# Performance work log

Measured on AMD Instinct MI355X. Metric: run time of the kernel, lower is better.

## Reference

```python
import jax, jax.numpy as jnp
import numpy as np

B, T, D, H = 1, 4096, 1024, 16
DK = D // H
SCALE = 1.0 / float(np.sqrt(DK))
NEG = -1e9


def setup_inputs() -> dict:
    key = jax.random.key(0)
    k1, k2, k3 = jax.random.split(key, 3)
    x = jax.random.normal(k1, (B, T, D), dtype=jnp.float32)
    # xavier-ish small weights (gain 0.5)
    Wqkv = jax.random.normal(k2, (3 * D, D), dtype=jnp.float32) * 0.02
    Wout = jax.random.normal(k3, (D, D), dtype=jnp.float32) * 0.02
    return {"x": x, "Wqkv": Wqkv, "Wout": Wout}


def reference(x, Wqkv, Wout):
    b, t, d = x.shape
    # QKV projection (no bias): [B,T,3D] -> [3,B,H,T,DK]
    qkv = jnp.einsum('btd,ed->bte', x, Wqkv)
    qkv = qkv.reshape(b, t, 3, H, DK).transpose(2, 0, 3, 1, 4)
    q, k, v = qkv[0], qkv[1], qkv[2]
    # scaled dot-product scores, clamped
    scores = jnp.einsum('bhtd,bhsd->bhts', q, k) * SCALE
    scores = jnp.clip(scores, -10.0, 10.0)
    # causal additive mask (strict upper triangle gets -1e9)
    mask = jnp.triu(jnp.full((t, t), NEG, dtype=scores.dtype), k=1)
    scores = scores + mask[None, None, :, :]
    attn = jax.nn.softmax(scores, axis=-1)  # dropout is identity in eval
    out = jnp.einsum('bhts,bhsd->bhtd', attn, v)
    out = out.transpose(0, 2, 1, 3).reshape(b, t, d)
    return jnp.einsum('btd,ed->bte', out, Wout)
```

## Files before the change

kernel.cpp:

```cpp
#include <hip/hip_runtime.h>

#define T_SEQ   4096
#define D_MODEL 1024
#define NH      16
#define HD      64
#define E3      3072
#define QSCL    0.125f
#define TILEB   (64L*E3)
#define SLOTSZ  16896
#define P0CAP   800

using u32x2  = __attribute__((ext_vector_type(2))) unsigned int;
using u32x4  = __attribute__((ext_vector_type(4))) unsigned int;
using u16x4  = __attribute__((ext_vector_type(4))) unsigned short;
using u16x8  = __attribute__((ext_vector_type(8))) unsigned short;
using u64x2  = __attribute__((ext_vector_type(2))) unsigned long long;
using f32x4  = __attribute__((ext_vector_type(4))) float;
using bf16x8 = __attribute__((ext_vector_type(8))) __bf16;

__device__ __forceinline__ unsigned short f2bf(float f){
  unsigned int u = __builtin_bit_cast(unsigned int, f);
  u += 0x7fffu + ((u >> 16) & 1u);
  return (unsigned short)(u >> 16);
}
__device__ __forceinline__ float bf2f(unsigned short v){
  unsigned int u = ((unsigned int)v) << 16;
  return __builtin_bit_cast(float, u);
}

__device__ __forceinline__ void gload_lds16(const void* g, void* l){
  __builtin_amdgcn_global_load_lds((const __attribute__((address_space(1))) void*)g,
                                   (__attribute__((address_space(3))) void*)l, 16, 0, 0);
}

__device__ __forceinline__ char* part_ptr(char* p0, char* p1, int slot){
  return (slot < P0CAP) ? p0 + (size_t)slot * SLOTSZ
                        : p1 + (size_t)(slot - P0CAP) * SLOTSZ;
}

#define XN4   (T_SEQ*D_MODEL/4)
#define WQN4  (E3*D_MODEL/4)
#define WON4  (D_MODEL*D_MODEL/4)
__global__ __launch_bounds__(256) void cvt_all(const float4* __restrict__ x,
                                               const float4* __restrict__ wq,
                                               const float4* __restrict__ wo,
                                               u16x4* __restrict__ xb,
                                               u16x4* __restrict__ wqb,
                                               u16x4* __restrict__ wob){
  int i = blockIdx.x * 256 + threadIdx.x;
  const float4* src; u16x4* dst; int j;
  if(i < XN4){ src = x;  dst = xb;  j = i; }
  else if(i < XN4 + WQN4){ src = wq; dst = wqb; j = i - XN4; }
  else { src = wo; dst = wob; j = i - XN4 - WQN4; }
  float4 v = src[j];
  u16x4 o = { f2bf(v.x), f2bf(v.y), f2bf(v.z), f2bf(v.w) };
  dst[j] = o;
}

template<int OUT_BF16, int QSCALE>
__global__ __launch_bounds__(256) void gemm_bt(const unsigned short* __restrict__ A,
                                               const unsigned short* __restrict__ B,
                                               void* __restrict__ Cv,
                                               int M, int N, int K){
  __shared__ unsigned short As[128*64];
  __shared__ unsigned short Bs[128*64];
  const int t    = threadIdx.x;
  const int lane = t & 63;
  const int w    = t >> 6;
  const int cc   = lane & 15;
  const int gg   = lane >> 4;

  const int nbx  = N >> 7;
  const int cpx  = gridDim.x >> 3;
  const int wg   = (blockIdx.x & 7) * cpx + (blockIdx.x >> 3);
  const int brow = (wg / nbx) * 128;
  const int bcol = (wg % nbx) * 128;
  const int wrow = (w >> 1) * 64;
  const int wcol = (w & 1) * 64;

  f32x4 acc[4][4];
  #pragma unroll
  for(int m=0;m<4;++m)
    #pragma unroll
    for(int n=0;n<4;++n)
      acc[m][n] = (f32x4){0.f,0.f,0.f,0.f};

  const int  srow = t >> 3;
  const int  schk = ((t & 7) ^ (srow & 7)) * 8;
  const long aBase = (long)(brow + srow) * K + schk;
  const long bBase = (long)(bcol + srow) * K + schk;

  const int kOff0 = cc*128 + (((gg    ) ^ (cc&7)) << 4);
  const int kOff1 = cc*128 + (((gg + 4) ^ (cc&7)) << 4);

  for(int k0 = 0; k0 < K; k0 += 64){
    __syncthreads();
    #pragma unroll
    for(int p=0;p<4;++p){
      gload_lds16(A + aBase + k0 + (long)p*32*K, (char*)As + p*4096 + t*16);
      gload_lds16(B + bBase + k0 + (long)p*32*K, (char*)Bs + p*4096 + t*16);
    }
    __syncthreads();

    #pragma unroll
    for(int kk=0;kk<2;++kk){
      const int off = kk ? kOff1 : kOff0;
      bf16x8 af[4], bfr[4];
      #pragma unroll
      for(int m=0;m<4;++m)
        af[m]  = *(const bf16x8*)((const char*)As + wrow*128 + m*2048 + off);
      #pragma unroll
      for(int n=0;n<4;++n)
        bfr[n] = *(const bf16x8*)((const char*)Bs + wcol*128 + n*2048 + off);
      #pragma unroll
      for(int m=0;m<4;++m)
        #pragma unroll
        for(int n=0;n<4;++n)
          acc[m][n] = __builtin_amdgcn_mfma_f32_16x16x32_bf16(af[m], bfr[n], acc[m][n], 0, 0, 0);
    }
  }

  #pragma unroll
  for(int m=0;m<4;++m){
    #pragma unroll
    for(int n=0;n<4;++n){
      const int row0 = brow + wrow + m*16 + gg*4;
      const int col  = bcol + wcol + n*16 + cc;
      const float sc = (QSCALE && col < D_MODEL) ? QSCL : 1.0f;
      #pragma unroll
      for(int r=0;r<4;++r){
        if constexpr (OUT_BF16 != 0){
          ((unsigned short*)Cv)[(long)(row0 + r)*N + col] = f2bf(acc[m][n][r] * sc);
        } else {
          ((float*)Cv)[(long)(row0 + r)*N + col] = acc[m][n][r];
        }
      }
    }
  }
}

__global__ __launch_bounds__(256) void gemm_bt64(const unsigned short* __restrict__ A,
                                                 const unsigned short* __restrict__ B,
                                                 float* __restrict__ C,
                                                 int M, int N, int K){
  __shared__ unsigned short As[64*64];
  __shared__ unsigned short Bs[128*64];
  const int t    = threadIdx.x;
  const int lane = t & 63;
  const int w    = t >> 6;
  const int cc   = lane & 15;
  const int gg   = lane >> 4;

  const int nbx  = N >> 7;
  const int cpx  = gridDim.x >> 3;
  const int wg   = (blockIdx.x & 7) * cpx + (blockIdx.x >> 3);
  const int brow = (wg / nbx) * 64;
  const int bcol = (wg % nbx) * 128;
  const int wrow = (w >> 1) * 32;
  const int wcol = (w & 1) * 64;

  f32x4 acc[2][4];
  #pragma unroll
  for(int m=0;m<2;++m)
    #pragma unroll
    for(int n=0;n<4;++n)
      acc[m][n] = (f32x4){0.f,0.f,0.f,0.f};

  const int  srow = t >> 3;
  const int  schk = ((t & 7) ^ (srow & 7)) * 8;
  const long aBase = (long)(brow + srow) * K + schk;
  const long bBase = (long)(bcol + srow) * K + schk;

  const int kOff0 = cc*128 + (((gg    ) ^ (cc&7)) << 4);
  const int kOff1 = cc*128 + (((gg + 4) ^ (cc&7)) << 4);

  for(int k0 = 0; k0 < K; k0 += 64){
    __syncthreads();
    #pragma unroll
    for(int p=0;p<2;++p)
      gload_lds16(A + aBase + k0 + (long)p*32*K, (char*)As + p*4096 + t*16);
    #pragma unroll
    for(int p=0;p<4;++p)
      gload_lds16(B + bBase + k0 + (long)p*32*K, (char*)Bs + p*4096 + t*16);
    __syncthreads();

    #pragma unroll
    for(int kk=0;kk<2;++kk){
      const int off = kk ? kOff1 : kOff0;
      bf16x8 af[2], bfr[4];
      #pragma unroll
      for(int m=0;m<2;++m)
        af[m]  = *(const bf16x8*)((const char*)As + wrow*128 + m*2048 + off);
      #pragma unroll
      for(int n=0;n<4;++n)
        bfr[n] = *(const bf16x8*)((const char*)Bs + wcol*128 + n*2048 + off);
      #pragma unroll
      for(int m=0;m<2;++m)
        #pragma unroll
        for(int n=0;n<4;++n)
          acc[m][n] = __builtin_amdgcn_mfma_f32_16x16x32_bf16(af[m], bfr[n], acc[m][n], 0, 0, 0);
    }
  }

  #pragma unroll
  for(int m=0;m<2;++m){
    #pragma unroll
    for(int n=0;n<4;++n){
      const int row0 = brow + wrow + m*16 + gg*4;
      const int col  = bcol + wcol + n*16 + cc;
      #pragma unroll
      for(int r=0;r<4;++r)
        C[(long)(row0 + r)*N + col] = acc[m][n][r];
    }
  }
}

__global__ __launch_bounds__(256, 3) void attn_part(const unsigned short* __restrict__ qkv,
                                                    unsigned short* __restrict__ attnb,
                                                    char* __restrict__ parts0,
                                                    char* __restrict__ parts1){
  __shared__ char LB[32768];

  const int t    = threadIdx.x;
  const int lane = t & 63;
  const int w    = t >> 6;
  const int cc   = lane & 15;
  const int gg   = lane >> 4;

  const int bid  = blockIdx.x;
  const int hd   = bid & 15;
  const int o_   = bid >> 4;

  int QB, t0, n, slot;
  if(o_ < 16){
    QB = 15 - (o_ >> 1); const int hf = o_ & 1;
    const int h0 = QB + 1;
    t0 = hf * h0; n = h0;
    slot = (hd*8 + (QB-8))*2 + hf;
  } else if(o_ < 24){
    QB = 23 - o_; t0 = 0; n = 2*QB + 2; slot = -1;
  } else if(o_ < 56){
    const int i = o_ - 24; QB = 23 - (i >> 2); const int qt = i & 3;
    const int n0 = 2*QB + 2, bsz = n0 >> 2, rem = n0 & 3;
    t0 = qt*bsz + (qt < rem ? qt : rem);
    n  = bsz + (qt < rem ? 1 : 0);
    slot = 256 + (hd*8 + (QB-16))*4 + qt;
  } else {
    const int i = o_ - 56; QB = 31 - (i >> 3); const int qt = i & 7;
    const int n0 = 2*QB + 2, bsz = n0 >> 3, rem = n0 & 7;
    t0 = qt*bsz + (qt < rem ? qt : rem);
    n  = bsz + (qt < rem ? 1 : 0);
    slot = 768 + (hd*8 + (QB-24))*8 + qt;
  }
  const int gA = 2*QB;
  const int qA = QB*128 + w*16;

  bf16x8 bqA0 = *(const bf16x8*)(qkv + (long)(qA+cc)*E3 + hd*HD +      gg*8);
  bf16x8 bqA1 = *(const bf16x8*)(qkv + (long)(qA+cc)*E3 + hd*HD + 32 + gg*8);
  bf16x8 bqB0 = *(const bf16x8*)(qkv + (long)(qA+64+cc)*E3 + hd*HD +      gg*8);
  bf16x8 bqB1 = *(const bf16x8*)(qkv + (long)(qA+64+cc)*E3 + hd*HD + 32 + gg*8);

  const f32x4 z4 = (f32x4){0.f,0.f,0.f,0.f};
  f32x4 accA0=z4, accA1=z4, accA2=z4, accA3=z4;
  f32x4 accB0=z4, accB1=z4, accB2=z4, accB3=z4;
  float rsA = 0.f, rsB = 0.f;

  const bool lb0 = (4*gg + 0) > cc;
  const bool lb1 = (4*gg + 1) > cc;
  const bool lb2 = (4*gg + 2) > cc;
  const bool lb3 = (4*gg + 3) > cc;

  const int kOffA = cc*128 + (((gg    ) ^ (cc&7)) << 4);
  const int kOffB = cc*128 + (((gg + 4) ^ (cc&7)) << 4);

  const unsigned ldsBase = (unsigned)(unsigned long long)(&LB[0]);
  const unsigned vA0 = ldsBase + 8192  + lane*8;
  const unsigned vA1 = ldsBase + 24576 + lane*8;

  const int kLane0 = (t>>3)*E3 + D_MODEL + hd*HD + (((t&7) ^ ((t>>3)&7)) << 3);
  const int kLane1 = kLane0 + 32*E3;
  const int vLane0 = (4*((t>>3)&15) + ((t&7)>>1))*E3 + 2*D_MODEL + hd*HD
                     + ((2*(t>>7) + (t&1)) << 3);
  const int vLane1 = vLane0 + 32;

  #define STAGE(g_, BUF) do{                                                       \
    const unsigned short* gb_ = qkv + (long)(g_)*TILEB;                            \
    gload_lds16(gb_ + kLane0, LB + (BUF)*16384 + t*16);                            \
    gload_lds16(gb_ + kLane1, LB + (BUF)*16384 + 4096  + t*16);                    \
    gload_lds16(gb_ + vLane0, LB + (BUF)*16384 + 8192  + t*16);                    \
    gload_lds16(gb_ + vLane1, LB + (BUF)*16384 + 12288 + t*16);                    \
  }while(0)

  #define TRRD(d_, va_, OFF_)                                                      \
    asm volatile("ds_read_b64_tr_b16 %0, %1 offset:%c2"                            \
                 : "=v"(d_) : "v"(va_), "i"(OFF_))

  #define PVHALF(vab_, HOFF, doA_, doB_)                                           \
  {                                                                                \
    unsigned long long q0_,q1_,q2_,q3_,q4_,q5_,q6_,q7_;                            \
    TRRD(q0_, vab_, (HOFF) + 0);    TRRD(q1_, vab_, (HOFF) + 512);                 \
    TRRD(q2_, vab_, (HOFF) + 2048); TRRD(q3_, vab_, (HOFF) + 2560);                \
    TRRD(q4_, vab_, (HOFF) + 4096); TRRD(q5_, vab_, (HOFF) + 4608);                \
    TRRD(q6_, vab_, (HOFF) + 6144); TRRD(q7_, vab_, (HOFF) + 6656);                \
    asm volatile("s_waitcnt lgkmcnt(0)");                                          \
    __builtin_amdgcn_sched_barrier(0);                                             \
    u64x2 w0_ = {q0_,q1_}; bf16x8 bv0_ = __builtin_bit_cast(bf16x8, w0_);          \
    u64x2 w1_ = {q2_,q3_}; bf16x8 bv1_ = __builtin_bit_cast(bf16x8, w1_);          \
    u64x2 w2_ = {q4_,q5_}; bf16x8 bv2_ = __builtin_bit_cast(bf16x8, w2_);          \
    u64x2 w3_ = {q6_,q7_}; bf16x8 bv3_ = __builtin_bit_cast(bf16x8, w3_);          \
    if(doA_){                                                                      \
      accA0 = __builtin_amdgcn_mfma_f32_16x16x32_bf16(paA_, bv0_, accA0, 0,0,0);   \
      accA1 = __builtin_amdgcn_mfma_f32_16x16x32_bf16(paA_, bv1_, accA1, 0,0,0);   \
      accA2 = __builtin_amdgcn_mfma_f32_16x16x32_bf16(paA_, bv2_, accA2, 0,0,0);   \
      accA3 = __builtin_amdgcn_mfma_f32_16x16x32_bf16(paA_, bv3_, accA3, 0,0,0);   \
    }                                                                              \
    if(doB_){                                                                      \
      accB0 = __builtin_amdgcn_mfma_f32_16x16x32_bf16(paB_, bv0_, accB0, 0,0,0);   \
      accB1 = __builtin_amdgcn_mfma_f32_16x16x32_bf16(paB_, bv1_, accB1, 0,0,0);   \
      accB2 = __builtin_amdgcn_mfma_f32_16x16x32_bf16(paB_, bv2_, accB2, 0,0,0);   \
      accB3 = __builtin_amdgcn_mfma_f32_16x16x32_bf16(paB_, bv3_, accB3, 0,0,0);   \
    }                                                                              \
  }

  #define PACK4(pk_) (bf16x8){ (__bf16)pk_[0][0],(__bf16)pk_[0][1],(__bf16)pk_[0][2],\
    (__bf16)pk_[0][3],(__bf16)pk_[1][0],(__bf16)pk_[1][1],(__bf16)pk_[1][2],        \
    (__bf16)pk_[1][3] }
  #define PACK4H(pk_) (bf16x8){ (__bf16)pk_[2][0],(__bf16)pk_[2][1],(__bf16)pk_[2][2],\
    (__bf16)pk_[2][3],(__bf16)pk_[3][0],(__bf16)pk_[3][1],(__bf16)pk_[3][2],        \
    (__bf16)pk_[3][3] }

  #define TILE_INT(g_, BUF)                                                        \
  {                                                                                \
    STAGE((g_)+1, (BUF)^1);                                                        \
    const char* kb_ = (const char*)LB + (BUF)*16384;                               \
    float pkA[4][4], pkB[4][4];                                                    \
    _Pragma("unroll")                                                              \
    for(int kt=0; kt<4; ++kt){                                                     \
      bf16x8 a0 = *(const bf16x8*)(kb_ + kOffA + kt*2048);                         \
      bf16x8 a1 = *(const bf16x8*)(kb_ + kOffB + kt*2048);                         \
      f32x4 sA = __builtin_amdgcn_mfma_f32_16x16x32_bf16(a0, bqA0, z4, 0,0,0);     \
      sA = __builtin_amdgcn_mfma_f32_16x16x32_bf16(a1, bqA1, sA, 0,0,0);           \
      f32x4 sB = __builtin_amdgcn_mfma_f32_16x16x32_bf16(a0, bqB0, z4, 0,0,0);     \
      sB = __builtin_amdgcn_mfma_f32_16x16x32_bf16(a1, bqB1, sB, 0,0,0);           \
      _Pragma("unroll")                                                            \
      for(int rr=0; rr<4; ++rr){                                                   \
        float pA_ = __expf(__builtin_amdgcn_fmed3f(sA[rr], -10.f, 10.f));          \
        float pB_ = __expf(__builtin_amdgcn_fmed3f(sB[rr], -10.f, 10.f));          \
        rsA += pA_; rsB += pB_;                                                    \
        pkA[kt][rr] = pA_; pkB[kt][rr] = pB_;                                      \
      }                                                                            \
    }                                                                              \
    bf16x8 paA_, paB_;                                                             \
    const unsigned vab_ = (BUF) ? vA1 : vA0;                                       \
    paA_ = PACK4(pkA);  paB_ = PACK4(pkB);                                         \
    PVHALF(vab_, 0, 1, 1);                                                         \
    paA_ = PACK4H(pkA); paB_ = PACK4H(pkB);                                        \
    PVHALF(vab_, 1024, 1, 1);                                                      \
    __syncthreads();                                                               \
  }

  #define TILE_TAIL(g_, BUFR)                                                      \
  {                                                                                \
    STAGE((g_)+1, (BUFR)^1);                                                       \
    const char* kb_ = (const char*)LB + (BUFR)*16384;                              \
    float pkA[4][4], pkB[4][4];                                                    \
    const bool dA_ = ((g_) == gA);                                                 \
    _Pragma("unroll")                                                              \
    for(int kt=0; kt<4; ++kt){                                                     \
      bf16x8 a0 = *(const bf16x8*)(kb_ + kOffA + kt*2048);                         \
      bf16x8 a1 = *(const bf16x8*)(kb_ + kOffB + kt*2048);                         \
      if(dA_){                                                                     \
        f32x4 sB = __builtin_amdgcn_mfma_f32_16x16x32_bf16(a0, bqB0, z4, 0,0,0);   \
        sB = __builtin_amdgcn_mfma_f32_16x16x32_bf16(a1, bqB1, sB, 0,0,0);         \
        _Pragma("unroll")                                                          \
        for(int rr=0; rr<4; ++rr){                                                 \
          float pB_ = __expf(__builtin_amdgcn_fmed3f(sB[rr], -10.f, 10.f));        \
          rsB += pB_; pkB[kt][rr] = pB_;                                           \
        }                                                                          \
        if(kt <= w){                                                               \
          f32x4 sA = __builtin_amdgcn_mfma_f32_16x16x32_bf16(a0, bqA0, z4, 0,0,0); \
          sA = __builtin_amdgcn_mfma_f32_16x16x32_bf16(a1, bqA1, sA, 0,0,0);       \
          float p0_ = __expf(__builtin_amdgcn_fmed3f(sA[0], -10.f, 10.f));         \
          float p1_ = __expf(__builtin_amdgcn_fmed3f(sA[1], -10.f, 10.f));         \
          float p2_ = __expf(__builtin_amdgcn_fmed3f(sA[2], -10.f, 10.f));         \
          float p3_ = __expf(__builtin_amdgcn_fmed3f(sA[3], -10.f, 10.f));         \
          if(kt == w){                                                             \
            p0_ = lb0 ? 0.f : p0_;  p1_ = lb1 ? 0.f : p1_;                         \
            p2_ = lb2 ? 0.f : p2_;  p3_ = lb3 ? 0.f : p3_;                         \
          }                                                                        \
          rsA += p0_ + p1_ + p2_ + p3_;                                            \
          pkA[kt][0]=p0_; pkA[kt][1]=p1_; pkA[kt][2]=p2_; pkA[kt][3]=p3_;          \
        } else {                                                                   \
          pkA[kt][0]=0.f; pkA[kt][1]=0.f; pkA[kt][2]=0.f; pkA[kt][3]=0.f;          \
        }                                                                          \
      } else {                                                                     \
        pkA[kt][0]=0.f; pkA[kt][1]=0.f; pkA[kt][2]=0.f; pkA[kt][3]=0.f;            \
        if(kt <= w){                                                               \
          f32x4 sB = __builtin_amdgcn_mfma_f32_16x16x32_bf16(a0, bqB0, z4, 0,0,0); \
          sB = __builtin_amdgcn_mfma_f32_16x16x32_bf16(a1, bqB1, sB, 0,0,0);       \
          float p0_ = __expf(__builtin_amdgcn_fmed3f(sB[0], -10.f, 10.f));         \
          float p1_ = __expf(__builtin_amdgcn_fmed3f(sB[1], -10.f, 10.f));         \
          float p2_ = __expf(__builtin_amdgcn_fmed3f(sB[2], -10.f, 10.f));         \
          float p3_ = __expf(__builtin_amdgcn_fmed3f(sB[3], -10.f, 10.f));         \
          if(kt == w){                                                             \
            p0_ = lb0 ? 0.f : p0_;  p1_ = lb1 ? 0.f : p1_;                         \
            p2_ = lb2 ? 0.f : p2_;  p3_ = lb3 ? 0.f : p3_;                         \
          }                                                                        \
          rsB += p0_ + p1_ + p2_ + p3_;                                            \
          pkB[kt][0]=p0_; pkB[kt][1]=p1_; pkB[kt][2]=p2_; pkB[kt][3]=p3_;          \
        } else {                                                                   \
          pkB[kt][0]=0.f; pkB[kt][1]=0.f; pkB[kt][2]=0.f; pkB[kt][3]=0.f;          \
        }                                                                          \
      }                                                                            \
    }                                                                              \
    bf16x8 paA_, paB_;                                                             \
    const unsigned vab_ = (BUFR) ? vA1 : vA0;                                      \
    paA_ = PACK4(pkA);  paB_ = PACK4(pkB);                                         \
    PVHALF(vab_, 0, dA_, 1);                                                       \
    paA_ = PACK4H(pkA); paB_ = PACK4H(pkB);                                        \
    if(w >= 2){ PVHALF(vab_, 1024, dA_, 1); }                                      \
    else if(dA_){ PVHALF(vab_, 1024, 0, 1); }                                      \
    __syncthreads();                                                               \
  }

  STAGE(t0, 0);
  __syncthreads();

  const int gap  = gA - t0;
  const int nInt = (n < gap) ? n : (gap < 0 ? 0 : gap);
  int lt = 0;
  while(lt + 2 <= nInt){
    TILE_INT(t0+lt,   0);
    TILE_INT(t0+lt+1, 1);
    lt += 2;
  }
  if(lt < nInt){ TILE_INT(t0+lt, 0); ++lt; }
  if(lt < n){ TILE_TAIL(t0+lt, (lt&1)); ++lt; }
  if(lt < n){ TILE_TAIL(t0+lt, (lt&1)); ++lt; }

  rsA += __shfl_xor(rsA, 16);  rsA += __shfl_xor(rsA, 32);
  rsB += __shfl_xor(rsB, 16);  rsB += __shfl_xor(rsB, 32);

  if(slot < 0){
    #pragma unroll
    for(int rr=0;rr<4;++rr){
      const float invA = 1.0f / __shfl(rsA, 4*gg + rr);
      const int rowA = qA + 4*gg + rr;
      unsigned short* dA = attnb + (long)rowA*D_MODEL + hd*HD + cc;
      dA[0]  = __builtin_bit_cast(unsigned short, (__bf16)(accA0[rr]*invA));
      dA[16] = __builtin_bit_cast(unsigned short, (__bf16)(accA1[rr]*invA));
      dA[32] = __builtin_bit_cast(unsigned short, (__bf16)(accA2[rr]*invA));
      dA[48] = __builtin_bit_cast(unsigned short, (__bf16)(accA3[rr]*invA));
      const float invB = 1.0f / __shfl(rsB, 4*gg + rr);
      unsigned short* dB = dA + 64L*D_MODEL;
      dB[0]  = __builtin_bit_cast(unsigned short, (__bf16)(accB0[rr]*invB));
      dB[16] = __builtin_bit_cast(unsigned short, (__bf16)(accB1[rr]*invB));
      dB[32] = __builtin_bit_cast(unsigned short, (__bf16)(accB2[rr]*invB));
      dB[48] = __builtin_bit_cast(unsigned short, (__bf16)(accB3[rr]*invB));
    }
  } else {
    char* sp = part_ptr(parts0, parts1, slot);
    #pragma unroll
    for(int rr=0;rr<4;++rr){
      const int rowA = w*16 + 4*gg + rr;
      unsigned short* dA = (unsigned short*)sp + rowA*64 + cc;
      dA[0]  = f2bf(accA0[rr]);
      dA[16] = f2bf(accA1[rr]);
      dA[32] = f2bf(accA2[rr]);
      dA[48] = f2bf(accA3[rr]);
      unsigned short* dB = dA + 64*64;
      dB[0]  = f2bf(accB0[rr]);
      dB[16] = f2bf(accB1[rr]);
      dB[32] = f2bf(accB2[rr]);
      dB[48] = f2bf(accB3[rr]);
    }
    if(gg == 0){
      ((float*)(sp + 16384))[w*16 + cc]      = rsA;
      ((float*)(sp + 16384))[64 + w*16 + cc] = rsB;
    }
  }
  #undef STAGE
  #undef TRRD
  #undef PVHALF
  #undef PACK4
  #undef PACK4H
  #undef TILE_INT
  #undef TILE_TAIL
}

__global__ __launch_bounds__(256) void attn_combine(char* __restrict__ parts0,
                                                    char* __restrict__ parts1,
                                                    unsigned short* __restrict__ attnb){
  const int b  = blockIdx.x;
  const int hd = b & 15;
  const int QB = 8 + (b >> 4);
  const int t  = threadIdx.x;
  const int r  = t >> 1;
  const int d0 = (t & 1) * 32;

  int s0_, np;
  if(QB < 16)      { s0_ = (hd*8 + (QB-8))*2;         np = 2; }
  else if(QB < 24) { s0_ = 256 + (hd*8 + (QB-16))*4;  np = 4; }
  else             { s0_ = 768 + (hd*8 + (QB-24))*8;  np = 8; }

  float rs = 0.f;
  float o[32];
  #pragma unroll
  for(int j=0;j<32;++j) o[j] = 0.f;

  for(int pi = 0; pi < np; ++pi){
    const char* pp = part_ptr(parts0, parts1, s0_ + pi);
    rs += ((const float*)(pp + 16384))[r];
    #pragma unroll
    for(int q=0;q<4;++q){
      u16x8 a = *(const u16x8*)(pp + (r*64 + d0 + q*8)*2);
      #pragma unroll
      for(int j=0;j<8;++j) o[q*8+j] += bf2f(a[j]);
    }
  }
  const float inv = 1.0f / rs;
  unsigned short* dst = attnb + (long)(QB*128 + r)*D_MODEL + hd*HD + d0;
  #pragma unroll
  for(int q=0;q<4;++q){
    u16x8 ov;
    #pragma unroll
    for(int j=0;j<8;++j) ov[j] = f2bf(o[q*8+j]*inv);
    *(u16x8*)(dst + q*8) = ov;
  }
}

extern "C" void kernel_launch(void* const* d_in, const int* in_sizes, int n_in,
                              void* d_out, int out_size, void* d_ws, size_t ws_size,
                              hipStream_t stream){
  (void)in_sizes; (void)n_in; (void)out_size; (void)ws_size;
  const float* x    = (const float*)d_in[0];
  const float* wqkv = (const float*)d_in[1];
  const float* wout = (const float*)d_in[2];
  char* ws = (char*)d_ws;
  unsigned short* woutb = (unsigned short*)(ws);
  unsigned short* attnb = (unsigned short*)(ws + (2u  << 20));
  unsigned short* qkvb  = (unsigned short*)(ws + (10u << 20));
  unsigned short* xb    = (unsigned short*)(ws + (34u << 20));
  unsigned short* wqkvb = (unsigned short*)(ws + (42u << 20));
  char*           parts0 = ws + (34u << 20);
  char*           parts1 = (char*)d_out;
  float* out = (float*)d_out;

  cvt_all<<<dim3((XN4 + WQN4 + WON4)/256), 256, 0, stream>>>(
      (const float4*)x, (const float4*)wqkv, (const float4*)wout,
      (u16x4*)xb, (u16x4*)wqkvb, (u16x4*)woutb);

  gemm_bt<1,1><<<dim3((T_SEQ/128)*(E3/128)), 256, 0, stream>>>(xb, wqkvb, qkvb, T_SEQ, E3, D_MODEL);

  attn_part<<<dim3(120*NH), 256, 0, stream>>>(qkvb, attnb, parts0, parts1);
  attn_combine<<<dim3(24*NH), 256, 0, stream>>>(parts0, parts1, attnb);

  gemm_bt64<<<dim3((T_SEQ/64)*(D_MODEL/128)), 256, 0, stream>>>(attnb, woutb, out, T_SEQ, D_MODEL, D_MODEL);
}
```

Measured before the change: 114.6 us.

## Triple-buffer K/V tiles in attention with prefetch distance two and counted waits

Grows shared memory to three 16KB buffers and stages the K/V tile two iterations ahead instead of one. A rotating buffer index replaces the fixed ping-pong. The full __syncthreads is replaced by s_waitcnt vmcnt(4) plus s_barrier, so the most recent prefetch can stay in flight across the barrier. This is meant to hide global-load latency better, at the cost of 48KB LDS per block, which may reduce occupancy below the 3 blocks per CU requested by launch_bounds. It also issues prefetches past the end of the tile range.

```diff
diff --git a/kernel.cpp b/kernel.cpp
--- a/kernel.cpp
+++ b/kernel.cpp
@@ -219,7 +219,7 @@
                                                     unsigned short* __restrict__ attnb,
                                                     char* __restrict__ parts0,
                                                     char* __restrict__ parts1){
-  __shared__ char LB[32768];
+  __shared__ char LB[49152];
 
   const int t    = threadIdx.x;
   const int lane = t & 63;
@@ -274,14 +274,15 @@
   const int kOffB = cc*128 + (((gg + 4) ^ (cc&7)) << 4);
 
   const unsigned ldsBase = (unsigned)(unsigned long long)(&LB[0]);
-  const unsigned vA0 = ldsBase + 8192  + lane*8;
-  const unsigned vA1 = ldsBase + 24576 + lane*8;
+  const unsigned vBase = ldsBase + 8192 + lane*8;
 
   const int kLane0 = (t>>3)*E3 + D_MODEL + hd*HD + (((t&7) ^ ((t>>3)&7)) << 3);
   const int kLane1 = kLane0 + 32*E3;
   const int vLane0 = (4*((t>>3)&15) + ((t&7)>>1))*E3 + 2*D_MODEL + hd*HD
                      + ((2*(t>>7) + (t&1)) << 3);
   const int vLane1 = vLane0 + 32;
+
+  int bufc = 0;
 
   #define STAGE(g_, BUF) do{                                                       \
     const unsigned short* gb_ = qkv + (long)(g_)*TILEB;                            \
@@ -289,6 +290,14 @@
     gload_lds16(gb_ + kLane1, LB + (BUF)*16384 + 4096  + t*16);                    \
     gload_lds16(gb_ + vLane0, LB + (BUF)*16384 + 8192  + t*16);                    \
     gload_lds16(gb_ + vLane1, LB + (BUF)*16384 + 12288 + t*16);                    \
+  }while(0)
+
+  #define BARRIER_CNT() do{                                                        \
+    __builtin_amdgcn_sched_barrier(0);                                             \
+    asm volatile("s_waitcnt vmcnt(4) lgkmcnt(0)" ::: "memory");                    \
+    __builtin_amdgcn_s_barrier();                                                  \
+    __builtin_amdgcn_sched_barrier(0);                                             \
+    bufc = (bufc == 2) ? 0 : bufc + 1;                                             \
   }while(0)
 
   #define TRRD(d_, va_, OFF_)                                                      \
@@ -329,10 +338,11 @@
     (__bf16)pk_[2][3],(__bf16)pk_[3][0],(__bf16)pk_[3][1],(__bf16)pk_[3][2],        \
     (__bf16)pk_[3][3] }
 
-  #define TILE_INT(g_, BUF)                                                        \
+  #define TILE_INT(g_)                                                             \
   {                                                                                \
-    STAGE((g_)+1, (BUF)^1);                                                        \
-    const char* kb_ = (const char*)LB + (BUF)*16384;                               \
+    const int bn2_ = (bufc >= 1) ? (bufc - 1) : 2;                 \
+    STAGE((g_)+2, bn2_);                                                           \
+    const char* kb_ = (const char*)LB + bufc*16384;                                \
     float pkA[4][4], pkB[4][4];                                                    \
     _Pragma("unroll")                                                              \
     for(int kt=0; kt<4; ++kt){                                                     \
@@ -351,18 +361,19 @@
       }                                                                            \
     }                                                                              \
     bf16x8 paA_, paB_;                                                             \
-    const unsigned vab_ = (BUF) ? vA1 : vA0;                                       \
+    const unsigned vab_ = vBase + bufc*16384;                                      \
     paA_ = PACK4(pkA);  paB_ = PACK4(pkB);                                         \
     PVHALF(vab_, 0, 1, 1);                                                         \
     paA_ = PACK4H(pkA); paB_ = PACK4H(pkB);                                        \
     PVHALF(vab_, 1024, 1, 1);                                                      \
-    __syncthreads();                                                               \
-  }
-
-  #define TILE_TAIL(g_, BUFR)                                                      \
+    BARRIER_CNT();                                                                 \
+  }
+
+  #define TILE_TAIL(g_)                                                            \
   {                                                                                \
-    STAGE((g_)+1, (BUFR)^1);                                                       \
-    const char* kb_ = (const char*)LB + (BUFR)*16384;                              \
+    const int bn2_ = (bufc >= 1) ? (bufc - 1) : 2;                                 \
+    STAGE((g_)+2, bn2_);                                                           \
+    const char* kb_ = (const char*)LB + bufc*16384;                                \
     float pkA[4][4], pkB[4][4];                                                    \
     const bool dA_ = ((g_) == gA);                                                 \
     _Pragma("unroll")                                                              \
@@ -414,29 +425,28 @@
       }                                                                            \
     }                                                                              \
     bf16x8 paA_, paB_;                                                             \
-    const unsigned vab_ = (BUFR) ? vA1 : vA0;                                      \
+    const unsigned vab_ = vBase + bufc*16384;                                      \
     paA_ = PACK4(pkA);  paB_ = PACK4(pkB);                                         \
     PVHALF(vab_, 0, dA_, 1);                                                       \
     paA_ = PACK4H(pkA); paB_ = PACK4H(pkB);                                        \
     if(w >= 2){ PVHALF(vab_, 1024, dA_, 1); }                                      \
     else if(dA_){ PVHALF(vab_, 1024, 0, 1); }                                      \
-    __syncthreads();                                                               \
-  }
-
-  STAGE(t0, 0);
-  __syncthreads();
+    BARRIER_CNT();                                                                 \
+  }
+
+  STAGE(t0,   0);
+  STAGE(t0+1, 1);
+  __builtin_amdgcn_sched_barrier(0);
+  asm volatile("s_waitcnt vmcnt(0) lgkmcnt(0)" ::: "memory");
+  __builtin_amdgcn_s_barrier();
+  __builtin_amdgcn_sched_barrier(0);
 
   const int gap  = gA - t0;
   const int nInt = (n < gap) ? n : (gap < 0 ? 0 : gap);
   int lt = 0;
-  while(lt + 2 <= nInt){
-    TILE_INT(t0+lt,   0);
-    TILE_INT(t0+lt+1, 1);
-    lt += 2;
-  }
-  if(lt < nInt){ TILE_INT(t0+lt, 0); ++lt; }
-  if(lt < n){ TILE_TAIL(t0+lt, (lt&1)); ++lt; }
-  if(lt < n){ TILE_TAIL(t0+lt, (lt&1)); ++lt; }
+  for(; lt < nInt; ++lt) TILE_INT(t0+lt);
+  if(lt < n){ TILE_TAIL(t0+lt); ++lt; }
+  if(lt < n){ TILE_TAIL(t0+lt); ++lt; }
 
   rsA += __shfl_xor(rsA, 16);  rsA += __shfl_xor(rsA, 32);
   rsB += __shfl_xor(rsB, 16);  rsB += __shfl_xor(rsB, 32);
@@ -480,6 +490,7 @@
     }
   }
   #undef STAGE
+  #undef BARRIER_CNT
   #undef TRRD
   #undef PVHALF
   #undef PACK4
```

Result: no change. 116.5 us (+1.7%).
